# Kernel tuning notes

Measured on AMD Instinct MI355X. Metric: run time of the kernel, lower is better.

Reference implementation:

```python
import jax, jax.numpy as jnp
import numpy as np
from jax import lax

B, T, I, H, L = 512, 2048, 16, 40, 3

def setup_inputs() -> dict:
    key = jax.random.key(0)
    ks = jax.random.split(key, 4 * L + 3)
    bound = 1.0 / np.sqrt(H)
    u = lambda k, shp: jax.random.uniform(k, shp, jnp.float32, -bound, bound)
    inp = {"x": jax.random.normal(ks[0], (B, T, I), jnp.float32)}
    for l in range(L):
        in_dim = I if l == 0 else H
        inp[f"w_ih{l}"] = u(ks[1 + 4 * l], (H, in_dim))
        inp[f"w_hh{l}"] = u(ks[2 + 4 * l], (H, H))
        inp[f"b_ih{l}"] = u(ks[3 + 4 * l], (H,))
        inp[f"b_hh{l}"] = u(ks[4 + 4 * l], (H,))
    inp["fc_w"] = u(ks[4 * L + 1], (1, H))
    inp["fc_b"] = u(ks[4 * L + 2], (1,))
    return inp

def _rnn_layer(x_seq, w_ih, w_hh, b_ih, b_hh):
    # Precompute input projection as one big GEMM: [B, T, H]
    xp = jnp.einsum('bti,hi->bth', x_seq, w_ih) + b_ih + b_hh
    h0 = jnp.zeros((x_seq.shape[0], w_hh.shape[0]), x_seq.dtype)
    def step(h, xt):  # xt: [B, H]
        h = jnp.tanh(xt + h @ w_hh.T)
        return h, h
    _, ys = lax.scan(step, h0, jnp.swapaxes(xp, 0, 1))  # [T, B, H]
    return jnp.swapaxes(ys, 0, 1)  # [B, T, H]

def reference(x, w_ih0, w_hh0, b_ih0, b_hh0,
              w_ih1, w_hh1, b_ih1, b_hh1,
              w_ih2, w_hh2, b_ih2, b_hh2, fc_w, fc_b):
    # Multi-layer tanh RNN (eval mode: inter-layer and final dropout are identity)
    h = _rnn_layer(x, w_ih0, w_hh0, b_ih0, b_hh0)
    h = _rnn_layer(h, w_ih1, w_hh1, b_ih1, b_hh1)
    h = _rnn_layer(h, w_ih2, w_hh2, b_ih2, b_hh2)
    last = h[:, -1, :]                     # [B, H]
    out = last @ fc_w.T + fc_b             # [B, 1]
    return out[:, 0]                       # [B]
```

## Files before the change

### kernel.cpp

```cpp
#include <hip/hip_runtime.h>
#include <cstddef>
#include <cstdint>

#define B_ 512
#define T_ 2048
#define I_ 16
#define H_ 40

typedef __fp16 half_t;
typedef half_t h2 __attribute__((ext_vector_type(2)));
typedef float f4 __attribute__((ext_vector_type(4)));

__device__ __forceinline__ float fast_tanh(float x) {
  float e = __builtin_amdgcn_exp2f(x * 2.8853900817779268f);
  return 1.0f - 2.0f * __builtin_amdgcn_rcpf(e + 1.0f);
}

__device__ __forceinline__ float dot2(h2 a, h2 b, float c) {
  return __builtin_amdgcn_fdot2(a, b, c, false);
}

__device__ __forceinline__ h2 cvtpk_v(float lo, float hi) {
  h2 r;
  asm volatile("v_cvt_pkrtz_f16_f32 %0, %1, %2" : "=v"(r) : "v"(lo), "v"(hi));
  return r;
}

#define PIN(v) asm volatile("" : "+v"(v))

#define GLOAD16(R0, R1, R2, R3, P)                                  \
  asm volatile("global_load_dwordx4 %0, %4, off\n\t"                \
               "global_load_dwordx4 %1, %4, off offset:16\n\t"      \
               "global_load_dwordx4 %2, %4, off offset:32\n\t"      \
               "global_load_dwordx4 %3, %4, off offset:48"          \
               : "=&v"(R0), "=&v"(R1), "=&v"(R2), "=&v"(R3)         \
               : "v"(P))

#define WAITX(N)                                                    \
  do {                                                              \
    asm volatile("s_waitcnt vmcnt(" #N ")" ::: "memory");           \
    __builtin_amdgcn_sched_barrier(0);                              \
  } while (0)

#define LOADW(DST, SRC, STR, N2)                                    \
  _Pragma("unroll") for (int k = 0; k < (N2); ++k) {                \
    DST[k][0] = (half_t)SRC[jr * (STR) + 2 * k];                    \
    DST[k][1] = (half_t)SRC[jr * (STR) + 2 * k + 1];                \
    PIN(DST[k]);                                                    \
  }

#define BCAST(NH, PAIRS) do {                                       \
  int nb_ = __builtin_amdgcn_update_dpp(                            \
      0, __builtin_bit_cast(int, (NH)), 0xB1, 0xf, 0xf, false);     \
  h2 pk_ = __builtin_amdgcn_cvt_pkrtz((NH),                         \
      __builtin_bit_cast(float, nb_));                              \
  int pkb_ = __builtin_bit_cast(int, pk_);                          \
  _Pragma("unroll") for (int p = 0; p < H_ / 2; ++p)                \
    PAIRS[p] = __builtin_bit_cast(h2,                               \
        __builtin_amdgcn_readlane(pkb_, 2 * p));                    \
} while (0)

#define HDS(PAIRS, W, A0, A1, A2, A3)                               \
  _Pragma("unroll") for (int p = 0; p < 5; ++p) {                   \
    A0 = dot2(PAIRS[4 * p + 0], (W)[4 * p + 0], A0);                \
    A1 = dot2(PAIRS[4 * p + 1], (W)[4 * p + 1], A1);                \
    A2 = dot2(PAIRS[4 * p + 2], (W)[4 * p + 2], A2);                \
    A3 = dot2(PAIRS[4 * p + 3], (W)[4 * p + 3], A3);                \
  }

#define STEP(XH) do {                                               \
                                             \
  float a0 = bias0, a1 = 0.f, a2 = 0.f, a3 = 0.f;                   \
  a0 = dot2(XH[0], w0i[0], a0); a1 = dot2(XH[1], w0i[1], a1);       \
  a2 = dot2(XH[2], w0i[2], a2); a3 = dot2(XH[3], w0i[3], a3);       \
  a0 = dot2(XH[4], w0i[4], a0); a1 = dot2(XH[5], w0i[5], a1);       \
  a2 = dot2(XH[6], w0i[6], a2); a3 = dot2(XH[7], w0i[7], a3);       \
  HDS(hp0, w0h, a0, a1, a2, a3);                        \
  const float nh0 = fast_tanh((a0 + a1) + (a2 + a3));               \
  BCAST(nh0, hp0);                                                  \
                                             \
  float b0 = bias1, b1 = 0.f, b2 = 0.f, b3 = 0.f;                   \
  HDS(hp0, w1i, b0, b1, b2, b3);                        \
  HDS(hp1, w1h, b0, b1, b2, b3);                        \
  const float nh1 = fast_tanh((b0 + b1) + (b2 + b3));               \
  BCAST(nh1, hp1);                                                  \
                                             \
  float c0 = bias2, c1 = 0.f, c2 = 0.f, c3 = 0.f;                   \
  HDS(hp1, w2i, c0, c1, c2, c3);                        \
  HDS(hp2, w2h, c0, c1, c2, c3);                        \
  nh2v = fast_tanh((c0 + c1) + (c2 + c3));                          \
  BCAST(nh2v, hp2);                                                 \
} while (0)

#define PACKX(XH, R0, R1, R2, R3)                                   \
  do {                                                              \
    XH[0] = cvtpk_v(R0[0], R0[1]); XH[1] = cvtpk_v(R0[2], R0[3]);   \
    XH[2] = cvtpk_v(R1[0], R1[1]); XH[3] = cvtpk_v(R1[2], R1[3]);   \
    XH[4] = cvtpk_v(R2[0], R2[1]); XH[5] = cvtpk_v(R2[2], R2[3]);   \
    XH[6] = cvtpk_v(R3[0], R3[1]); XH[7] = cvtpk_v(R3[2], R3[3]);   \
  } while (0)

__global__ __launch_bounds__(64)
__attribute__((amdgpu_waves_per_eu(1, 1)))
void rnn3_fused(const float* __restrict__ x,
                const float* __restrict__ wih0, const float* __restrict__ whh0,
                const float* __restrict__ bih0, const float* __restrict__ bhh0,
                const float* __restrict__ wih1, const float* __restrict__ whh1,
                const float* __restrict__ b_ih1, const float* __restrict__ bhh1,
                const float* __restrict__ wih2, const float* __restrict__ whh2,
                const float* __restrict__ bih2, const float* __restrict__ bhh2,
                const float* __restrict__ fcw, const float* __restrict__ fcb,
                float* __restrict__ out) {
  const int b = blockIdx.x;
  const int j = threadIdx.x;
  const int jr = (j < H_) ? j : (H_ - 1);

  h2 w0i[I_ / 2], w0h[H_ / 2], w1i[H_ / 2], w1h[H_ / 2], w2i[H_ / 2], w2h[H_ / 2];
  LOADW(w0i, wih0, I_, I_ / 2)
  LOADW(w0h, whh0, H_, H_ / 2)
  LOADW(w1i, wih1, H_, H_ / 2)
  LOADW(w1h, whh1, H_, H_ / 2)
  LOADW(w2i, wih2, H_, H_ / 2)
  LOADW(w2h, whh2, H_, H_ / 2)

  float bias0 = bih0[jr] + bhh0[jr];  PIN(bias0);
  float bias1 = b_ih1[jr] + bhh1[jr]; PIN(bias1);
  float bias2 = bih2[jr] + bhh2[jr];  PIN(bias2);

  h2 hp0[H_ / 2], hp1[H_ / 2], hp2[H_ / 2];
#pragma unroll
  for (int p = 0; p < H_ / 2; ++p) {
    hp0[p] = h2{(half_t)0.f, (half_t)0.f};
    hp1[p] = h2{(half_t)0.f, (half_t)0.f};
    hp2[p] = h2{(half_t)0.f, (half_t)0.f};
  }

  const float* __restrict__ xb = x + (size_t)b * (T_ * I_);

  f4 rA0, rA1, rA2, rA3, rB0, rB1, rB2, rB3;
  GLOAD16(rA0, rA1, rA2, rA3, xb + 0 * I_);
  GLOAD16(rB0, rB1, rB2, rB3, xb + 1 * I_);

  float nh2v = 0.f;
  h2 xh[8];

  for (int t = 0; t < T_; t += 2) {
    WAITX(4);
    PACKX(xh, rA0, rA1, rA2, rA3);
    STEP(xh);
    { const float* pf = xb + (size_t)((t + 2 < T_) ? t + 2 : T_ - 1) * I_;
      GLOAD16(rA0, rA1, rA2, rA3, pf); }
    WAITX(4);
    PACKX(xh, rB0, rB1, rB2, rB3);
    STEP(xh);
    { const float* pf = xb + (size_t)((t + 3 < T_) ? t + 3 : T_ - 1) * I_;
      GLOAD16(rB0, rB1, rB2, rB3, pf); }
  }

  asm volatile("s_waitcnt vmcnt(0)" ::: "memory");
  __builtin_amdgcn_sched_barrier(0);
  PIN(rA0); PIN(rA1); PIN(rA2); PIN(rA3);
  PIN(rB0); PIN(rB1); PIN(rB2); PIN(rB3);

  const float fw = (j < H_) ? fcw[j] : 0.f;
  float v = nh2v * fw;
#pragma unroll
  for (int off = 32; off > 0; off >>= 1) v += __shfl_down(v, off);
  if (j == 0) out[b] = v + fcb[0];
}

extern "C" void kernel_launch(void* const* d_in, const int* in_sizes, int n_in,
                              void* d_out, int out_size, void* d_ws, size_t ws_size,
                              hipStream_t stream) {
  (void)in_sizes; (void)n_in; (void)d_ws; (void)ws_size; (void)out_size;
  const float* x    = (const float*)d_in[0];
  const float* wih0 = (const float*)d_in[1];
  const float* whh0 = (const float*)d_in[2];
  const float* bih0 = (const float*)d_in[3];
  const float* bhh0 = (const float*)d_in[4];
  const float* wih1 = (const float*)d_in[5];
  const float* whh1 = (const float*)d_in[6];
  const float* bih1 = (const float*)d_in[7];
  const float* bhh1 = (const float*)d_in[8];
  const float* wih2 = (const float*)d_in[9];
  const float* whh2 = (const float*)d_in[10];
  const float* bih2 = (const float*)d_in[11];
  const float* bhh2 = (const float*)d_in[12];
  const float* fcw  = (const float*)d_in[13];
  const float* fcb  = (const float*)d_in[14];
  float* out = (float*)d_out;

  hipLaunchKernelGGL(rnn3_fused, dim3(B_), dim3(64), 0, stream,
                     x, wih0, whh0, bih0, bhh0,
                     wih1, whh1, bih1, bhh1,
                     wih2, whh2, bih2, bhh2,
                     fcw, fcb, out);
}
```

Baseline: 926.3 us.

## Wavefront-pipeline the three RNN layers across three waves via LDS handoff

Assigns each RNN layer to its own wavefront in a 192-thread block and runs them as a layer-skewed pipeline. Each wave publishes its packed fp16 hidden state to a double-buffered LDS array for the next layer, with block barriers between ticks. The goal is to shorten the serial per-timestep critical path from three layers to roughly one. The cost is a __syncthreads plus LDS round-trip every tick, and three waves per block instead of one.

```diff
diff --git a/kernel.cpp b/kernel.cpp
--- a/kernel.cpp
+++ b/kernel.cpp
@@ -9,38 +9,31 @@
 
 typedef __fp16 half_t;
 typedef half_t h2 __attribute__((ext_vector_type(2)));
+typedef half_t h8 __attribute__((ext_vector_type(8)));
 typedef float f4 __attribute__((ext_vector_type(4)));
 
 __device__ __forceinline__ float fast_tanh(float x) {
   float e = __builtin_amdgcn_exp2f(x * 2.8853900817779268f);
   return 1.0f - 2.0f * __builtin_amdgcn_rcpf(e + 1.0f);
 }
-
 __device__ __forceinline__ float dot2(h2 a, h2 b, float c) {
   return __builtin_amdgcn_fdot2(a, b, c, false);
 }
-
 __device__ __forceinline__ h2 cvtpk_v(float lo, float hi) {
   h2 r;
   asm volatile("v_cvt_pkrtz_f16_f32 %0, %1, %2" : "=v"(r) : "v"(lo), "v"(hi));
   return r;
 }
-
 #define PIN(v) asm volatile("" : "+v"(v))
 
-#define GLOAD16(R0, R1, R2, R3, P)                                  \
+#define GLOADQ(R0, R1, R2, R3, P)                                   \
   asm volatile("global_load_dwordx4 %0, %4, off\n\t"                \
                "global_load_dwordx4 %1, %4, off offset:16\n\t"      \
                "global_load_dwordx4 %2, %4, off offset:32\n\t"      \
                "global_load_dwordx4 %3, %4, off offset:48"          \
                : "=&v"(R0), "=&v"(R1), "=&v"(R2), "=&v"(R3)         \
                : "v"(P))
-
-#define WAITX(N)                                                    \
-  do {                                                              \
-    asm volatile("s_waitcnt vmcnt(" #N ")" ::: "memory");           \
-    __builtin_amdgcn_sched_barrier(0);                              \
-  } while (0)
+#define WAITX(N) asm volatile("s_waitcnt vmcnt(" #N ")")
 
 #define LOADW(DST, SRC, STR, N2)                                    \
   _Pragma("unroll") for (int k = 0; k < (N2); ++k) {                \
@@ -49,12 +42,16 @@
     PIN(DST[k]);                                                    \
   }
 
-#define BCAST(NH, PAIRS) do {                                       \
+#define BCAST_PUB(NH, PAIRS, PUB, PH, LY) do {                      \
   int nb_ = __builtin_amdgcn_update_dpp(                            \
       0, __builtin_bit_cast(int, (NH)), 0xB1, 0xf, 0xf, false);     \
   h2 pk_ = __builtin_amdgcn_cvt_pkrtz((NH),                         \
       __builtin_bit_cast(float, nb_));                              \
   int pkb_ = __builtin_bit_cast(int, pk_);                          \
+  if (PUB) {                                                        \
+    if (((lane) & 1) == 0 && (lane) < H_)                           \
+      hbuf[PH][LY][(lane) >> 1] = (unsigned)pkb_;                   \
+  }                                                                 \
   _Pragma("unroll") for (int p = 0; p < H_ / 2; ++p)                \
     PAIRS[p] = __builtin_bit_cast(h2,                               \
         __builtin_amdgcn_readlane(pkb_, 2 * p));                    \
@@ -68,29 +65,15 @@
     A3 = dot2(PAIRS[4 * p + 3], (W)[4 * p + 3], A3);                \
   }
 
-#define STEP(XH) do {                                               \
-                                             \
-  float a0 = bias0, a1 = 0.f, a2 = 0.f, a3 = 0.f;                   \
-  a0 = dot2(XH[0], w0i[0], a0); a1 = dot2(XH[1], w0i[1], a1);       \
-  a2 = dot2(XH[2], w0i[2], a2); a3 = dot2(XH[3], w0i[3], a3);       \
-  a0 = dot2(XH[4], w0i[4], a0); a1 = dot2(XH[5], w0i[5], a1);       \
-  a2 = dot2(XH[6], w0i[6], a2); a3 = dot2(XH[7], w0i[7], a3);       \
-  HDS(hp0, w0h, a0, a1, a2, a3);                        \
-  const float nh0 = fast_tanh((a0 + a1) + (a2 + a3));               \
-  BCAST(nh0, hp0);                                                  \
-                                             \
-  float b0 = bias1, b1 = 0.f, b2 = 0.f, b3 = 0.f;                   \
-  HDS(hp0, w1i, b0, b1, b2, b3);                        \
-  HDS(hp1, w1h, b0, b1, b2, b3);                        \
-  const float nh1 = fast_tanh((b0 + b1) + (b2 + b3));               \
-  BCAST(nh1, hp1);                                                  \
-                                             \
-  float c0 = bias2, c1 = 0.f, c2 = 0.f, c3 = 0.f;                   \
-  HDS(hp1, w2i, c0, c1, c2, c3);                        \
-  HDS(hp2, w2h, c0, c1, c2, c3);                        \
-  nh2v = fast_tanh((c0 + c1) + (c2 + c3));                          \
-  BCAST(nh2v, hp2);                                                 \
-} while (0)
+#define HDQ(Q, W, A0, A1, A2, A3)                                   \
+  _Pragma("unroll") for (int m = 0; m < 5; ++m) {                   \
+    h2 p0 = {Q[m][0], Q[m][1]}, p1 = {Q[m][2], Q[m][3]};            \
+    h2 p2 = {Q[m][4], Q[m][5]}, p3 = {Q[m][6], Q[m][7]};            \
+    A0 = dot2(p0, (W)[4 * m + 0], A0);                              \
+    A1 = dot2(p1, (W)[4 * m + 1], A1);                              \
+    A2 = dot2(p2, (W)[4 * m + 2], A2);                              \
+    A3 = dot2(p3, (W)[4 * m + 3], A3);                              \
+  }
 
 #define PACKX(XH, R0, R1, R2, R3)                                   \
   do {                                                              \
@@ -100,8 +83,46 @@
     XH[6] = cvtpk_v(R3[0], R3[1]); XH[7] = cvtpk_v(R3[2], R3[3]);   \
   } while (0)
 
-__global__ __launch_bounds__(64)
-__attribute__((amdgpu_waves_per_eu(1, 1)))
+#define TICK_A(R0, R1, R2, R3, PH, TNEXT) do {                      \
+  WAITX(4);                                                         \
+  PACKX(xh, R0, R1, R2, R3);                                        \
+  float a0 = bias0, a1 = 0.f, a2 = 0.f, a3 = 0.f;                   \
+  a0 = dot2(xh[0], w0i[0], a0); a1 = dot2(xh[1], w0i[1], a1);       \
+  a2 = dot2(xh[2], w0i[2], a2); a3 = dot2(xh[3], w0i[3], a3);       \
+  a0 = dot2(xh[4], w0i[4], a0); a1 = dot2(xh[5], w0i[5], a1);       \
+  a2 = dot2(xh[6], w0i[6], a2); a3 = dot2(xh[7], w0i[7], a3);       \
+  HDS(hpA, w0h, a0, a1, a2, a3);                                    \
+  float nh0 = fast_tanh((a0 + a1) + (a2 + a3));                     \
+  BCAST_PUB(nh0, hpA, 1, PH, 0);                                    \
+  { const float* pf_ = xb +                                         \
+        (size_t)(((TNEXT) < T_) ? (TNEXT) : (T_ - 1)) * I_;         \
+    GLOADQ(R0, R1, R2, R3, pf_); }                                  \
+} while (0)
+
+#define TICK_B(PH, PHR) do {                                        \
+  h8 q[5];                                                          \
+  { const h8* hq_ = (const h8*)&hbuf[PHR][0][0];                    \
+    _Pragma("unroll") for (int m = 0; m < 5; ++m) q[m] = hq_[m]; }  \
+  float b0v = bias1, b1v = 0.f, b2v = 0.f, b3v = 0.f;               \
+  HDS(hpB, w1h, b0v, b1v, b2v, b3v);                                \
+  HDQ(q, w1i, b0v, b1v, b2v, b3v);                                  \
+  float nh1 = fast_tanh((b0v + b1v) + (b2v + b3v));                 \
+  BCAST_PUB(nh1, hpB, 1, PH, 1);                                    \
+} while (0)
+
+#define TICK_C(PHR) do {                                            \
+  h8 q[5];                                                          \
+  { const h8* hq_ = (const h8*)&hbuf[PHR][1][0];                    \
+    _Pragma("unroll") for (int m = 0; m < 5; ++m) q[m] = hq_[m]; }  \
+  float c0v = bias2, c1v = 0.f, c2v = 0.f, c3v = 0.f;               \
+  HDS(hpC, w2h, c0v, c1v, c2v, c3v);                                \
+  HDQ(q, w2i, c0v, c1v, c2v, c3v);                                  \
+  nh2v = fast_tanh((c0v + c1v) + (c2v + c3v));                      \
+  BCAST_PUB(nh2v, hpC, 0, 0, 0);                                    \
+} while (0)
+
+__global__ __launch_bounds__(192)
+__attribute__((amdgpu_waves_per_eu(2, 2)))
 void rnn3_fused(const float* __restrict__ x,
                 const float* __restrict__ wih0, const float* __restrict__ whh0,
                 const float* __restrict__ bih0, const float* __restrict__ bhh0,
@@ -112,61 +133,79 @@
                 const float* __restrict__ fcw, const float* __restrict__ fcb,
                 float* __restrict__ out) {
   const int b = blockIdx.x;
-  const int j = threadIdx.x;
-  const int jr = (j < H_) ? j : (H_ - 1);
-
-  h2 w0i[I_ / 2], w0h[H_ / 2], w1i[H_ / 2], w1h[H_ / 2], w2i[H_ / 2], w2h[H_ / 2];
-  LOADW(w0i, wih0, I_, I_ / 2)
-  LOADW(w0h, whh0, H_, H_ / 2)
-  LOADW(w1i, wih1, H_, H_ / 2)
-  LOADW(w1h, whh1, H_, H_ / 2)
-  LOADW(w2i, wih2, H_, H_ / 2)
-  LOADW(w2h, whh2, H_, H_ / 2)
-
-  float bias0 = bih0[jr] + bhh0[jr];  PIN(bias0);
-  float bias1 = b_ih1[jr] + bhh1[jr]; PIN(bias1);
-  float bias2 = bih2[jr] + bhh2[jr];  PIN(bias2);
-
-  h2 hp0[H_ / 2], hp1[H_ / 2], hp2[H_ / 2];
-#pragma unroll
-  for (int p = 0; p < H_ / 2; ++p) {
-    hp0[p] = h2{(half_t)0.f, (half_t)0.f};
-    hp1[p] = h2{(half_t)0.f, (half_t)0.f};
-    hp2[p] = h2{(half_t)0.f, (half_t)0.f};
-  }
-
+  const int lane = threadIdx.x & 63;
+  const int wv = threadIdx.x >> 6;
+  const int jr = (lane < H_) ? lane : (H_ - 1);
+
+  __shared__ __align__(16) unsigned hbuf[2][2][24];
+
+  h2 w0i[8], w0h[20], w1i[20], w1h[20], w2i[20], w2h[20];
+  h2 hpA[20], hpB[20], hpC[20];
+  float bias0 = 0.f, bias1 = 0.f, bias2 = 0.f;
+  f4 rA0, rA1, rA2, rA3, rB0, rB1, rB2, rB3;
+  h2 xh[8];
+  float nh2v = 0.f;
   const float* __restrict__ xb = x + (size_t)b * (T_ * I_);
 
-  f4 rA0, rA1, rA2, rA3, rB0, rB1, rB2, rB3;
-  GLOAD16(rA0, rA1, rA2, rA3, xb + 0 * I_);
-  GLOAD16(rB0, rB1, rB2, rB3, xb + 1 * I_);
-
-  float nh2v = 0.f;
-  h2 xh[8];
-
-  for (int t = 0; t < T_; t += 2) {
-    WAITX(4);
-    PACKX(xh, rA0, rA1, rA2, rA3);
-    STEP(xh);
-    { const float* pf = xb + (size_t)((t + 2 < T_) ? t + 2 : T_ - 1) * I_;
-      GLOAD16(rA0, rA1, rA2, rA3, pf); }
-    WAITX(4);
-    PACKX(xh, rB0, rB1, rB2, rB3);
-    STEP(xh);
-    { const float* pf = xb + (size_t)((t + 3 < T_) ? t + 3 : T_ - 1) * I_;
-      GLOAD16(rB0, rB1, rB2, rB3, pf); }
-  }
-
-  asm volatile("s_waitcnt vmcnt(0)" ::: "memory");
-  __builtin_amdgcn_sched_barrier(0);
-  PIN(rA0); PIN(rA1); PIN(rA2); PIN(rA3);
-  PIN(rB0); PIN(rB1); PIN(rB2); PIN(rB3);
-
-  const float fw = (j < H_) ? fcw[j] : 0.f;
-  float v = nh2v * fw;
-#pragma unroll
-  for (int off = 32; off > 0; off >>= 1) v += __shfl_down(v, off);
-  if (j == 0) out[b] = v + fcb[0];
+  if (wv == 0) {
+    LOADW(w0i, wih0, I_, 8)
+    LOADW(w0h, whh0, H_, 20)
+    bias0 = bih0[jr] + bhh0[jr]; PIN(bias0);
+#pragma unroll
+    for (int p = 0; p < 20; ++p) hpA[p] = h2{(half_t)0.f, (half_t)0.f};
+    GLOADQ(rA0, rA1, rA2, rA3, xb);
+    GLOADQ(rB0, rB1, rB2, rB3, xb + I_);
+  } else if (wv == 1) {
+    LOADW(w1i, wih1, H_, 20)
+    LOADW(w1h, whh1, H_, 20)
+    bias1 = b_ih1[jr] + bhh1[jr]; PIN(bias1);
+#pragma unroll
+    for (int p = 0; p < 20; ++p) hpB[p] = h2{(half_t)0.f, (half_t)0.f};
+  } else {
+    LOADW(w2i, wih2, H_, 20)
+    LOADW(w2h, whh2, H_, 20)
+    bias2 = bih2[jr] + bhh2[jr]; PIN(bias2);
+#pragma unroll
+    for (int p = 0; p < 20; ++p) hpC[p] = h2{(half_t)0.f, (half_t)0.f};
+  }
+  __syncthreads();
+
+  if (wv == 0) TICK_A(rA0, rA1, rA2, rA3, 0, 2);
+  __syncthreads();
+  if (wv == 0)      TICK_A(rB0, rB1, rB2, rB3, 1, 3);
+  else if (wv == 1) TICK_B(1, 0);
+  __syncthreads();
+
+  for (int u = 2; u < T_; u += 2) {
+    if (wv == 0)      TICK_A(rA0, rA1, rA2, rA3, 0, u + 2);
+    else if (wv == 1) TICK_B(0, 1);
+    else              TICK_C(1);
+    __syncthreads();
+    if (wv == 0)      TICK_A(rB0, rB1, rB2, rB3, 1, u + 3);
+    else if (wv == 1) TICK_B(1, 0);
+    else              TICK_C(0);
+    __syncthreads();
+  }
+
+  if (wv == 0) {
+    asm volatile("s_waitcnt vmcnt(0)");
+    PIN(rA0); PIN(rA1); PIN(rA2); PIN(rA3);
+    PIN(rB0); PIN(rB1); PIN(rB2); PIN(rB3);
+  } else if (wv == 1) {
+    TICK_B(0, 1);
+  } else {
+    TICK_C(1);
+  }
+  __syncthreads();
+
+  if (wv == 2) {
+    TICK_C(0);
+    const float fw = (lane < H_) ? fcw[lane] : 0.f;
+    float v = nh2v * fw;
+#pragma unroll
+    for (int off = 32; off > 0; off >>= 1) v += __shfl_down(v, off);
+    if (lane == 0) out[b] = v + fcb[0];
+  }
 }
 
 extern "C" void kernel_launch(void* const* d_in, const int* in_sizes, int n_in,
@@ -190,7 +229,7 @@
   const float* fcb  = (const float*)d_in[14];
   float* out = (float*)d_out;
 
-  hipLaunchKernelGGL(rnn3_fused, dim3(B_), dim3(64), 0, stream,
+  hipLaunchKernelGGL(rnn3_fused, dim3(B_), dim3(192), 0, stream,
                      x, wih0, whh0, bih0, bhh0,
                      wih1, whh1, bih1, bhh1,
                      wih2, whh2, bih2, bhh2,
```

Result: slower. 1.094 ms (+18.1%).

## Interleave two batch sequences per wave to overlap independent recurrence chains

Applied to the files above, without the earlier changes.

Each wave now processes two batch elements, alternating timesteps between them so their independent dependency chains can hide each other's latency. The grid is halved and the x prefetch is restructured into lo/hi quads for both sequences with deeper outstanding loads. This trades parallelism across CUs/SIMDs for instruction-level overlap within a wave, and raises register use.

```diff
diff --git a/kernel.cpp b/kernel.cpp
--- a/kernel.cpp
+++ b/kernel.cpp
@@ -15,32 +15,31 @@
   float e = __builtin_amdgcn_exp2f(x * 2.8853900817779268f);
   return 1.0f - 2.0f * __builtin_amdgcn_rcpf(e + 1.0f);
 }
-
 __device__ __forceinline__ float dot2(h2 a, h2 b, float c) {
   return __builtin_amdgcn_fdot2(a, b, c, false);
 }
-
 __device__ __forceinline__ h2 cvtpk_v(float lo, float hi) {
   h2 r;
   asm volatile("v_cvt_pkrtz_f16_f32 %0, %1, %2" : "=v"(r) : "v"(lo), "v"(hi));
   return r;
 }
-
 #define PIN(v) asm volatile("" : "+v"(v))
 
-#define GLOAD16(R0, R1, R2, R3, P)                                  \
+#define GLOADQ_LO(R0, R1, R2, R3, P)                                \
   asm volatile("global_load_dwordx4 %0, %4, off\n\t"                \
                "global_load_dwordx4 %1, %4, off offset:16\n\t"      \
                "global_load_dwordx4 %2, %4, off offset:32\n\t"      \
                "global_load_dwordx4 %3, %4, off offset:48"          \
                : "=&v"(R0), "=&v"(R1), "=&v"(R2), "=&v"(R3)         \
                : "v"(P))
-
-#define WAITX(N)                                                    \
-  do {                                                              \
-    asm volatile("s_waitcnt vmcnt(" #N ")" ::: "memory");           \
-    __builtin_amdgcn_sched_barrier(0);                              \
-  } while (0)
+#define GLOADQ_HI(R0, R1, R2, R3, P)                                \
+  asm volatile("global_load_dwordx4 %0, %4, off offset:64\n\t"      \
+               "global_load_dwordx4 %1, %4, off offset:80\n\t"      \
+               "global_load_dwordx4 %2, %4, off offset:96\n\t"      \
+               "global_load_dwordx4 %3, %4, off offset:112"         \
+               : "=&v"(R0), "=&v"(R1), "=&v"(R2), "=&v"(R3)         \
+               : "v"(P))
+#define WAITX(N) asm volatile("s_waitcnt vmcnt(" #N ")")
 
 #define LOADW(DST, SRC, STR, N2)                                    \
   _Pragma("unroll") for (int k = 0; k < (N2); ++k) {                \
@@ -68,28 +67,25 @@
     A3 = dot2(PAIRS[4 * p + 3], (W)[4 * p + 3], A3);                \
   }
 
-#define STEP(XH) do {                                               \
-                                             \
+#define STEP(XH, HP0, HP1, HP2, NH2V) do {                          \
   float a0 = bias0, a1 = 0.f, a2 = 0.f, a3 = 0.f;                   \
   a0 = dot2(XH[0], w0i[0], a0); a1 = dot2(XH[1], w0i[1], a1);       \
   a2 = dot2(XH[2], w0i[2], a2); a3 = dot2(XH[3], w0i[3], a3);       \
   a0 = dot2(XH[4], w0i[4], a0); a1 = dot2(XH[5], w0i[5], a1);       \
   a2 = dot2(XH[6], w0i[6], a2); a3 = dot2(XH[7], w0i[7], a3);       \
-  HDS(hp0, w0h, a0, a1, a2, a3);                        \
+  HDS(HP0, w0h, a0, a1, a2, a3);                                    \
   const float nh0 = fast_tanh((a0 + a1) + (a2 + a3));               \
-  BCAST(nh0, hp0);                                                  \
-                                             \
-  float b0 = bias1, b1 = 0.f, b2 = 0.f, b3 = 0.f;                   \
-  HDS(hp0, w1i, b0, b1, b2, b3);                        \
-  HDS(hp1, w1h, b0, b1, b2, b3);                        \
-  const float nh1 = fast_tanh((b0 + b1) + (b2 + b3));               \
-  BCAST(nh1, hp1);                                                  \
-                                             \
-  float c0 = bias2, c1 = 0.f, c2 = 0.f, c3 = 0.f;                   \
-  HDS(hp1, w2i, c0, c1, c2, c3);                        \
-  HDS(hp2, w2h, c0, c1, c2, c3);                        \
-  nh2v = fast_tanh((c0 + c1) + (c2 + c3));                          \
-  BCAST(nh2v, hp2);                                                 \
+  BCAST(nh0, HP0);                                                  \
+  float b0v = bias1, b1v = 0.f, b2v = 0.f, b3v = 0.f;               \
+  HDS(HP0, w1i, b0v, b1v, b2v, b3v);                    \
+  HDS(HP1, w1h, b0v, b1v, b2v, b3v);                    \
+  const float nh1 = fast_tanh((b0v + b1v) + (b2v + b3v));           \
+  BCAST(nh1, HP1);                                                  \
+  float c0v = bias2, c1v = 0.f, c2v = 0.f, c3v = 0.f;               \
+  HDS(HP1, w2i, c0v, c1v, c2v, c3v);                    \
+  HDS(HP2, w2h, c0v, c1v, c2v, c3v);                    \
+  NH2V = fast_tanh((c0v + c1v) + (c2v + c3v));                      \
+  BCAST(NH2V, HP2);                                                 \
 } while (0)
 
 #define PACKX(XH, R0, R1, R2, R3)                                   \
@@ -111,7 +107,7 @@
                 const float* __restrict__ bih2, const float* __restrict__ bhh2,
                 const float* __restrict__ fcw, const float* __restrict__ fcb,
                 float* __restrict__ out) {
-  const int b = blockIdx.x;
+  const int b0 = 2 * blockIdx.x;
   const int j = threadIdx.x;
   const int jr = (j < H_) ? j : (H_ - 1);
 
@@ -127,46 +123,70 @@
   float bias1 = b_ih1[jr] + bhh1[jr]; PIN(bias1);
   float bias2 = bih2[jr] + bhh2[jr];  PIN(bias2);
 
-  h2 hp0[H_ / 2], hp1[H_ / 2], hp2[H_ / 2];
+  h2 hpA0[20], hpA1[20], hpA2[20], hpB0[20], hpB1[20], hpB2[20];
 #pragma unroll
-  for (int p = 0; p < H_ / 2; ++p) {
-    hp0[p] = h2{(half_t)0.f, (half_t)0.f};
-    hp1[p] = h2{(half_t)0.f, (half_t)0.f};
-    hp2[p] = h2{(half_t)0.f, (half_t)0.f};
-  }
-
-  const float* __restrict__ xb = x + (size_t)b * (T_ * I_);
-
-  f4 rA0, rA1, rA2, rA3, rB0, rB1, rB2, rB3;
-  GLOAD16(rA0, rA1, rA2, rA3, xb + 0 * I_);
-  GLOAD16(rB0, rB1, rB2, rB3, xb + 1 * I_);
-
-  float nh2v = 0.f;
+  for (int p = 0; p < 20; ++p) {
+    hpA0[p] = h2{(half_t)0.f, (half_t)0.f}; hpA1[p] = hpA0[p]; hpA2[p] = hpA0[p];
+    hpB0[p] = hpA0[p]; hpB1[p] = hpA0[p]; hpB2[p] = hpA0[p];
+  }
+
+  const float* __restrict__ xb0 = x + (size_t)b0 * (T_ * I_);
+  const float* __restrict__ xb1 = xb0 + (size_t)(T_ * I_);
+
+  f4 a00, a01, a02, a03, a10, a11, a12, a13;
+  f4 c00, c01, c02, c03, c10, c11, c12, c13;
+  GLOADQ_LO(a00, a01, a02, a03, xb0);
+  GLOADQ_LO(c00, c01, c02, c03, xb1);
+  GLOADQ_HI(a10, a11, a12, a13, xb0);
+  GLOADQ_HI(c10, c11, c12, c13, xb1);
+
+  float nh2A = 0.f, nh2B = 0.f;
   h2 xh[8];
 
   for (int t = 0; t < T_; t += 2) {
-    WAITX(4);
-    PACKX(xh, rA0, rA1, rA2, rA3);
-    STEP(xh);
-    { const float* pf = xb + (size_t)((t + 2 < T_) ? t + 2 : T_ - 1) * I_;
-      GLOAD16(rA0, rA1, rA2, rA3, pf); }
-    WAITX(4);
-    PACKX(xh, rB0, rB1, rB2, rB3);
-    STEP(xh);
-    { const float* pf = xb + (size_t)((t + 3 < T_) ? t + 3 : T_ - 1) * I_;
-      GLOAD16(rB0, rB1, rB2, rB3, pf); }
-  }
-
-  asm volatile("s_waitcnt vmcnt(0)" ::: "memory");
-  __builtin_amdgcn_sched_barrier(0);
-  PIN(rA0); PIN(rA1); PIN(rA2); PIN(rA3);
-  PIN(rB0); PIN(rB1); PIN(rB2); PIN(rB3);
+    const float* pf0 = xb0 + (size_t)((t + 2 < T_) ? (t + 2) : (T_ - 2)) * I_;
+    const float* pf1 = xb1 + (size_t)((t + 2 < T_) ? (t + 2) : (T_ - 2)) * I_;
+
+    WAITX(12);
+    PACKX(xh, a00, a01, a02, a03);
+    STEP(xh, hpA0, hpA1, hpA2, nh2A);
+    GLOADQ_LO(a00, a01, a02, a03, pf0);
+
+    WAITX(12);
+    PACKX(xh, c00, c01, c02, c03);
+    STEP(xh, hpB0, hpB1, hpB2, nh2B);
+    GLOADQ_LO(c00, c01, c02, c03, pf1);
+
+    WAITX(12);
+    PACKX(xh, a10, a11, a12, a13);
+    STEP(xh, hpA0, hpA1, hpA2, nh2A);
+    GLOADQ_HI(a10, a11, a12, a13, pf0);
+
+    WAITX(12);
+    PACKX(xh, c10, c11, c12, c13);
+    STEP(xh, hpB0, hpB1, hpB2, nh2B);
+    GLOADQ_HI(c10, c11, c12, c13, pf1);
+  }
+
+  asm volatile("s_waitcnt vmcnt(0)");
+  PIN(a00); PIN(a01); PIN(a02); PIN(a03);
+  PIN(a10); PIN(a11); PIN(a12); PIN(a13);
+  PIN(c00); PIN(c01); PIN(c02); PIN(c03);
+  PIN(c10); PIN(c11); PIN(c12); PIN(c13);
 
   const float fw = (j < H_) ? fcw[j] : 0.f;
-  float v = nh2v * fw;
+  float va = nh2A * fw;
+  float vb = nh2B * fw;
 #pragma unroll
-  for (int off = 32; off > 0; off >>= 1) v += __shfl_down(v, off);
-  if (j == 0) out[b] = v + fcb[0];
+  for (int off = 32; off > 0; off >>= 1) {
+    va += __shfl_down(va, off);
+    vb += __shfl_down(vb, off);
+  }
+  if (j == 0) {
+    const float fb = fcb[0];
+    out[b0]     = va + fb;
+    out[b0 + 1] = vb + fb;
+  }
 }
 
 extern "C" void kernel_launch(void* const* d_in, const int* in_sizes, int n_in,
@@ -190,7 +210,7 @@
   const float* fcb  = (const float*)d_in[14];
   float* out = (float*)d_out;
 
-  hipLaunchKernelGGL(rnn3_fused, dim3(B_), dim3(64), 0, stream,
+  hipLaunchKernelGGL(rnn3_fused, dim3(B_ / 2), dim3(64), 0, stream,
                      x, wih0, whh0, bih0, bhh0,
                      wih1, whh1, bih1, bhh1,
                      wih2, whh2, bih2, bhh2,
```

New measurement: 1.914 ms. +106.7%, slower.
